# Optimization experiments

Hardware: AMD Instinct MI355X
Metric: run time of the kernel (lower is better)

The kernel has to match this reference:

```python
import jax, jax.numpy as jnp
import numpy as np

N = 1024
C = 50000
D = 128
M_MARGIN = 0.35
S_SCALE = 30.0
LAMDA = 0.01


def setup_inputs() -> dict:
    key = jax.random.key(0)
    k1, k2, k3 = jax.random.split(key, 3)
    feature = jax.random.normal(k1, (N, D), dtype=jnp.float32)
    weight = jax.random.normal(k2, (C, D), dtype=jnp.float32)
    label = jax.random.randint(k3, (N,), 0, C, dtype=jnp.int64)
    return {"feature": feature, "weight": weight, "label": label}


def reference(feature, weight, label):
    eps = 1e-8  # torch CosineSimilarity eps
    f = feature / jnp.maximum(jnp.linalg.norm(feature, axis=-1, keepdims=True), eps)
    w = weight / jnp.maximum(jnp.linalg.norm(weight, axis=-1, keepdims=True), eps)
    cos = jnp.einsum("nd,cd->nc", f, w)  # [N, C] cosine similarities
    onehot = jax.nn.one_hot(label, C, dtype=cos.dtype)  # [N, C]
    # CosFace: subtract margin m from the target-class cosine, scale by s
    logits = S_SCALE * (cos - M_MARGIN * onehot)
    target_logit = S_SCALE * (jnp.take_along_axis(cos, label[:, None], axis=1)[:, 0] - M_MARGIN)
    # -log( exp(t) / (exp(t) + sum_{j != y} exp(s*cos_j)) ) = logsumexp(logits) - t
    lse = jax.nn.logsumexp(logits, axis=-1)  # [N]
    loss_lmc = jnp.mean(lse - target_logit)
    # center loss: 0.5 * sum_i ||f_i - w_{y_i}||^2
    diff = feature - weight[label]
    loss_c = 0.5 * jnp.sum(diff * diff)
    return loss_lmc + LAMDA * loss_c
```

## Files before the change

kernel.cpp:

```cpp
#include <hip/hip_runtime.h>

#define N_ROWS   1024
#define D_DIM    128
#define C_CLS    50000
#define C_PAD    50048
#define NCT64    782
#define NG       96
#define NPART    192
#define S_SCALE  30.0f
#define M_MARGIN 0.35f
#define EXP2_SCALE 43.2808512266689f

typedef short s8v __attribute__((ext_vector_type(8)));
typedef float f4v __attribute__((ext_vector_type(4)));

__device__ inline unsigned short f2bf(float f) {
    unsigned u = __float_as_uint(f);
    u += 0x7FFF + ((u >> 16) & 1);
    return (unsigned short)(u >> 16);
}
__device__ inline float bf2f(unsigned short h) {
    return __uint_as_float(((unsigned)h) << 16);
}
__device__ inline void load_lds16(const char* src, unsigned char* lds) {
    __builtin_amdgcn_global_load_lds(
        (const __attribute__((address_space(1))) void*)src,
        (__attribute__((address_space(3))) void*)lds, 16, 0, 0);
}

__global__ void norm_rows_fused(const float* __restrict__ weight,
                                const float* __restrict__ feature,
                                unsigned short* __restrict__ what,
                                unsigned short* __restrict__ fhat) {
    int wid = threadIdx.x >> 6, lane = threadIdx.x & 63;
    int r = blockIdx.x * 4 + wid;
    const float* src;
    unsigned short* dst;
    int srcRow, valid;
    if (r < C_PAD) {
        src = weight; dst = what; srcRow = r; valid = (r < C_CLS);
    } else {
        src = feature; dst = fhat; srcRow = r - C_PAD; valid = 1;
    }
    float2 v = make_float2(0.f, 0.f);
    if (valid) v = ((const float2*)src)[(size_t)srcRow * 64 + lane];
    float ss = v.x * v.x + v.y * v.y;
    #pragma unroll
    for (int s = 1; s < 64; s <<= 1) ss += __shfl_xor(ss, s, 64);
    float inv = valid ? 1.0f / fmaxf(sqrtf(ss), 1e-8f) : 0.f;
    ((ushort2*)dst)[(size_t)srcRow * 64 + lane] =
        make_ushort2(f2bf(v.x * inv), f2bf(v.y * inv));
}

__global__ __launch_bounds__(256, 3)
void gemm_exp_kernel(const short* __restrict__ fhat,
                     const short* __restrict__ what,
                     float* __restrict__ part2) {
    __shared__ __align__(16) unsigned char smem[49152];
    const int g   = blockIdx.x;
    const int rt  = blockIdx.y;
    const int tid = threadIdx.x;
    const int wid = tid >> 6;
    const int lane = tid & 63;
    const int lrow = lane & 15;
    const int kgrp = lane >> 4;
    const int wrow = wid >> 1;
    const int wcol = wid & 1;
    const int nt = (g < 14) ? 9 : 8;

    const char* aSrc  = (const char*)fhat + (size_t)rt * 32768;
    const char* bBase = (const char*)what;

    #pragma unroll
    for (int i = 0; i < 8; i++) {
        int o = wid * 8192 + i * 1024 + lane * 16;
        int s = o ^ (((o >> 8) & 7) << 4);
        load_lds16(aSrc + s, smem + o);
    }
    __syncthreads();

    s8v afr[4][4];
    #pragma unroll
    for (int kk = 0; kk < 4; kk++)
        #pragma unroll
        for (int m = 0; m < 4; m++) {
            int row = wrow * 64 + m * 16 + lrow;
            int b = (row * 256 + kk * 64 + kgrp * 16) ^ ((row & 7) << 4);
            afr[kk][m] = *(const s8v*)(smem + b);
        }
    __syncthreads();

    #pragma unroll
    for (int i = 0; i < 4; i++) {
        int o = wid * 4096 + i * 1024 + lane * 16;
        int s = o ^ (((o >> 8) & 7) << 4);
        load_lds16(bBase + (size_t)g * 16384 + s, smem + o);
        load_lds16(bBase + (size_t)(g + 96) * 16384 + s, smem + 16384 + o);
    }

    float esum[4][4];
    #pragma unroll
    for (int m = 0; m < 4; m++)
        #pragma unroll
        for (int j = 0; j < 4; j++) esum[m][j] = 0.f;

    for (int t = 0; t < nt; ++t) {
        const int ct = g + 96 * t;
        if (t + 1 < nt) asm volatile("s_waitcnt vmcnt(4)" ::: "memory");
        else            asm volatile("s_waitcnt vmcnt(0)" ::: "memory");
        __builtin_amdgcn_s_barrier();
        __builtin_amdgcn_sched_barrier(0);

        if (t + 2 < nt) {
            const char* src = bBase + (size_t)(ct + 192) * 16384;
            unsigned char* dstb = smem + ((t + 2) % 3) * 16384;
            #pragma unroll
            for (int i = 0; i < 4; i++) {
                int o = wid * 4096 + i * 1024 + lane * 16;
                int s = o ^ (((o >> 8) & 7) << 4);
                load_lds16(src + s, dstb + o);
            }
        }

        const unsigned char* bb = smem + (t % 3) * 16384;
        f4v acc[4][2];
        f4v zero = {0.f, 0.f, 0.f, 0.f};
        #pragma unroll
        for (int m = 0; m < 4; m++) { acc[m][0] = zero; acc[m][1] = zero; }

        #pragma unroll
        for (int kk = 0; kk < 4; kk++) {
            s8v bfr[2];
            #pragma unroll
            for (int n = 0; n < 2; n++) {
                int row = wcol * 32 + n * 16 + lrow;
                int b = (row * 256 + kk * 64 + kgrp * 16) ^ ((row & 7) << 4);
                bfr[n] = *(const s8v*)(bb + b);
            }
            #pragma unroll
            for (int m = 0; m < 4; m++) {
                acc[m][0] = __builtin_amdgcn_mfma_f32_16x16x32_bf16(
                    afr[kk][m], bfr[0], acc[m][0], 0, 0, 0);
                acc[m][1] = __builtin_amdgcn_mfma_f32_16x16x32_bf16(
                    afr[kk][m], bfr[1], acc[m][1], 0, 0, 0);
            }
        }

        if (ct != NCT64 - 1) {
            #pragma unroll
            for (int m = 0; m < 4; m++)
                #pragma unroll
                for (int n = 0; n < 2; n++)
                    #pragma unroll
                    for (int j = 0; j < 4; j++)
                        esum[m][j] += __builtin_amdgcn_exp2f(EXP2_SCALE * acc[m][n][j]);
        } else {
            #pragma unroll
            for (int n = 0; n < 2; n++) {
                int gc = ct * 64 + wcol * 32 + n * 16 + lrow;
                #pragma unroll
                for (int m = 0; m < 4; m++)
                    #pragma unroll
                    for (int j = 0; j < 4; j++)
                        if (gc < C_CLS)
                            esum[m][j] += __builtin_amdgcn_exp2f(EXP2_SCALE * acc[m][n][j]);
            }
        }
    }

    #pragma unroll
    for (int m = 0; m < 4; m++)
        #pragma unroll
        for (int j = 0; j < 4; j++) {
            float v = esum[m][j];
            v += __shfl_xor(v, 1, 64);
            v += __shfl_xor(v, 2, 64);
            v += __shfl_xor(v, 4, 64);
            v += __shfl_xor(v, 8, 64);
            if (lrow == 0) {
                int row = rt * 128 + wrow * 64 + m * 16 + kgrp * 4 + j;
                part2[(size_t)row * NPART + g * 2 + wcol] = v;
            }
        }
}

__global__ void finalize_rows_kernel(const float* __restrict__ part2,
                                     const unsigned short* __restrict__ fhat,
                                     const unsigned short* __restrict__ what,
                                     const float* __restrict__ feature,
                                     const float* __restrict__ weight,
                                     const int* __restrict__ label,
                                     float* __restrict__ rowval) {
    int wid = threadIdx.x >> 6, lane = threadIdx.x & 63;
    int n = blockIdx.x * 4 + wid;
    int y = label[n];

    const float* p = part2 + (size_t)n * NPART;
    float S = p[lane] + p[64 + lane] + p[128 + lane];

    float2 f2 = ((const float2*)feature)[(size_t)n * 64 + lane];
    float2 w2 = ((const float2*)weight)[(size_t)y * 64 + lane];
    float dx = f2.x - w2.x, dy = f2.y - w2.y;
    float cl = dx * dx + dy * dy;

    ushort2 fh = ((const ushort2*)fhat)[(size_t)n * 64 + lane];
    ushort2 wh = ((const ushort2*)what)[(size_t)y * 64 + lane];
    float cy = bf2f(fh.x) * bf2f(wh.x) + bf2f(fh.y) * bf2f(wh.y);

    #pragma unroll
    for (int s = 1; s < 64; s <<= 1) {
        S  += __shfl_xor(S, s, 64);
        cl += __shfl_xor(cl, s, 64);
        cy += __shfl_xor(cy, s, 64);
    }
    if (lane == 0) {
        float t  = S_SCALE * (cy - M_MARGIN);
        float Sp = S - __expf(S_SCALE * cy) + __expf(t);
        rowval[n] = (logf(Sp) - t) * (1.0f / (float)N_ROWS) + 0.005f * cl;
    }
}

__global__ void reduce_final_kernel(const float* __restrict__ rowval, float* __restrict__ out) {
    __shared__ float sbuf[4];
    int t = threadIdx.x;
    float v = rowval[t] + rowval[t + 256] + rowval[t + 512] + rowval[t + 768];
    #pragma unroll
    for (int s = 1; s < 64; s <<= 1) v += __shfl_xor(v, s, 64);
    if ((t & 63) == 0) sbuf[t >> 6] = v;
    __syncthreads();
    if (t == 0) out[0] = sbuf[0] + sbuf[1] + sbuf[2] + sbuf[3];
}

extern "C" void kernel_launch(void* const* d_in, const int* in_sizes, int n_in,
                              void* d_out, int out_size, void* d_ws, size_t ws_size,
                              hipStream_t stream) {
    const float* feature = (const float*)d_in[0];
    const float* weight  = (const float*)d_in[1];
    const int*   label   = (const int*)d_in[2];

    const size_t WS_NEEDED = 13864960;
    if (ws_size < WS_NEEDED) return;

    char* ws = (char*)d_ws;
    unsigned short* what = (unsigned short*)ws;
    unsigned short* fhat = (unsigned short*)(ws + 12812288);
    float*         part2 = (float*)(ws + 13074432);
    float*        rowval = (float*)(ws + 13860864);

    norm_rows_fused<<<dim3((C_PAD + N_ROWS) / 4), 256, 0, stream>>>(weight, feature, what, fhat);
    gemm_exp_kernel<<<dim3(NG, 8), 256, 0, stream>>>((const short*)fhat, (const short*)what, part2);
    finalize_rows_kernel<<<dim3(N_ROWS / 4), 256, 0, stream>>>(part2, fhat, what, feature, weight,
                                                               label, rowval);
    reduce_final_kernel<<<1, 256, 0, stream>>>(rowval, (float*)d_out);
}
```

Before: 38.53 us.

## Widen GEMM grid to 128 groups with double buffering and prescaled features

The GEMM grid grows from 96 to 128 column groups, and the triple-buffered B pipeline with manual vmcnt waits becomes a double buffer using __syncthreads. This halves LDS from 48KB to 32KB, allowing occupancy 4 and more concurrent blocks. The exp2 scale is folded into the normalized features, removing a multiply per element, and the finalize step adapts to the scaled logits. The normalization kernel now handles two rows per wavefront using float4 loads. The trade-off is less prefetch depth (one tile ahead), which may expose memory latency.

```diff
diff --git a/kernel.cpp b/kernel.cpp
--- a/kernel.cpp
+++ b/kernel.cpp
@@ -5,11 +5,13 @@
 #define C_CLS    50000
 #define C_PAD    50048
 #define NCT64    782
-#define NG       96
-#define NPART    192
+#define NG       128
+#define NPART    256
 #define S_SCALE  30.0f
 #define M_MARGIN 0.35f
 #define EXP2_SCALE 43.2808512266689f
+#define EXP2M      15.1482979293341f
+#define LN2        0.6931471805599453f
 
 typedef short s8v __attribute__((ext_vector_type(8)));
 typedef float f4v __attribute__((ext_vector_type(4)));
@@ -33,30 +35,35 @@
                                 unsigned short* __restrict__ what,
                                 unsigned short* __restrict__ fhat) {
     int wid = threadIdx.x >> 6, lane = threadIdx.x & 63;
-    int r = blockIdx.x * 4 + wid;
+    int half = lane >> 5, l32 = lane & 31;
+    int r = blockIdx.x * 8 + wid * 2 + half;
+
     const float* src;
     unsigned short* dst;
     int srcRow, valid;
+    float scale;
     if (r < C_PAD) {
-        src = weight; dst = what; srcRow = r; valid = (r < C_CLS);
+        src = weight; dst = what; srcRow = r; valid = (r < C_CLS); scale = 1.0f;
     } else {
-        src = feature; dst = fhat; srcRow = r - C_PAD; valid = 1;
-    }
-    float2 v = make_float2(0.f, 0.f);
-    if (valid) v = ((const float2*)src)[(size_t)srcRow * 64 + lane];
-    float ss = v.x * v.x + v.y * v.y;
-    #pragma unroll
-    for (int s = 1; s < 64; s <<= 1) ss += __shfl_xor(ss, s, 64);
-    float inv = valid ? 1.0f / fmaxf(sqrtf(ss), 1e-8f) : 0.f;
-    ((ushort2*)dst)[(size_t)srcRow * 64 + lane] =
-        make_ushort2(f2bf(v.x * inv), f2bf(v.y * inv));
-}
-
-__global__ __launch_bounds__(256, 3)
+        src = feature; dst = fhat; srcRow = r - C_PAD; valid = 1; scale = EXP2_SCALE;
+    }
+    float4 v = make_float4(0.f, 0.f, 0.f, 0.f);
+    if (valid) v = ((const float4*)src)[(size_t)srcRow * 32 + l32];
+    float ss = v.x * v.x + v.y * v.y + v.z * v.z + v.w * v.w;
+    #pragma unroll
+    for (int s = 1; s < 32; s <<= 1) ss += __shfl_xor(ss, s, 32);
+    float inv = valid ? scale / fmaxf(sqrtf(ss), 1e-8f) : 0.f;
+    ushort4 o;
+    o.x = f2bf(v.x * inv); o.y = f2bf(v.y * inv);
+    o.z = f2bf(v.z * inv); o.w = f2bf(v.w * inv);
+    ((ushort4*)dst)[(size_t)srcRow * 32 + l32] = o;
+}
+
+__global__ __launch_bounds__(256, 4)
 void gemm_exp_kernel(const short* __restrict__ fhat,
                      const short* __restrict__ what,
                      float* __restrict__ part2) {
-    __shared__ __align__(16) unsigned char smem[49152];
+    __shared__ __align__(16) unsigned char smem[32768];
     const int g   = blockIdx.x;
     const int rt  = blockIdx.y;
     const int tid = threadIdx.x;
@@ -66,7 +73,7 @@
     const int kgrp = lane >> 4;
     const int wrow = wid >> 1;
     const int wcol = wid & 1;
-    const int nt = (g < 14) ? 9 : 8;
+    const int nt = (g < 14) ? 7 : 6;
 
     const char* aSrc  = (const char*)fhat + (size_t)rt * 32768;
     const char* bBase = (const char*)what;
@@ -95,7 +102,6 @@
         int o = wid * 4096 + i * 1024 + lane * 16;
         int s = o ^ (((o >> 8) & 7) << 4);
         load_lds16(bBase + (size_t)g * 16384 + s, smem + o);
-        load_lds16(bBase + (size_t)(g + 96) * 16384 + s, smem + 16384 + o);
     }
 
     float esum[4][4];
@@ -105,15 +111,12 @@
         for (int j = 0; j < 4; j++) esum[m][j] = 0.f;
 
     for (int t = 0; t < nt; ++t) {
-        const int ct = g + 96 * t;
-        if (t + 1 < nt) asm volatile("s_waitcnt vmcnt(4)" ::: "memory");
-        else            asm volatile("s_waitcnt vmcnt(0)" ::: "memory");
-        __builtin_amdgcn_s_barrier();
-        __builtin_amdgcn_sched_barrier(0);
-
-        if (t + 2 < nt) {
-            const char* src = bBase + (size_t)(ct + 192) * 16384;
-            unsigned char* dstb = smem + ((t + 2) % 3) * 16384;
+        const int ct = g + 128 * t;
+        __syncthreads();
+
+        if (t + 1 < nt) {
+            const char* src = bBase + (size_t)(ct + 128) * 16384;
+            unsigned char* dstb = smem + ((t + 1) & 1) * 16384;
             #pragma unroll
             for (int i = 0; i < 4; i++) {
                 int o = wid * 4096 + i * 1024 + lane * 16;
@@ -122,7 +125,7 @@
             }
         }
 
-        const unsigned char* bb = smem + (t % 3) * 16384;
+        const unsigned char* bb = smem + (t & 1) * 16384;
         f4v acc[4][2];
         f4v zero = {0.f, 0.f, 0.f, 0.f};
         #pragma unroll
@@ -153,7 +156,7 @@
                 for (int n = 0; n < 2; n++)
                     #pragma unroll
                     for (int j = 0; j < 4; j++)
-                        esum[m][j] += __builtin_amdgcn_exp2f(EXP2_SCALE * acc[m][n][j]);
+                        esum[m][j] += __builtin_amdgcn_exp2f(acc[m][n][j]);
         } else {
             #pragma unroll
             for (int n = 0; n < 2; n++) {
@@ -163,7 +166,7 @@
                     #pragma unroll
                     for (int j = 0; j < 4; j++)
                         if (gc < C_CLS)
-                            esum[m][j] += __builtin_amdgcn_exp2f(EXP2_SCALE * acc[m][n][j]);
+                            esum[m][j] += __builtin_amdgcn_exp2f(acc[m][n][j]);
             }
         }
     }
@@ -196,7 +199,7 @@
     int y = label[n];
 
     const float* p = part2 + (size_t)n * NPART;
-    float S = p[lane] + p[64 + lane] + p[128 + lane];
+    float S = p[lane] + p[64 + lane] + p[128 + lane] + p[192 + lane];
 
     float2 f2 = ((const float2*)feature)[(size_t)n * 64 + lane];
     float2 w2 = ((const float2*)weight)[(size_t)y * 64 + lane];
@@ -205,18 +208,18 @@
 
     ushort2 fh = ((const ushort2*)fhat)[(size_t)n * 64 + lane];
     ushort2 wh = ((const ushort2*)what)[(size_t)y * 64 + lane];
-    float cy = bf2f(fh.x) * bf2f(wh.x) + bf2f(fh.y) * bf2f(wh.y);
+    float cys = bf2f(fh.x) * bf2f(wh.x) + bf2f(fh.y) * bf2f(wh.y);
 
     #pragma unroll
     for (int s = 1; s < 64; s <<= 1) {
-        S  += __shfl_xor(S, s, 64);
-        cl += __shfl_xor(cl, s, 64);
-        cy += __shfl_xor(cy, s, 64);
+        S   += __shfl_xor(S, s, 64);
+        cl  += __shfl_xor(cl, s, 64);
+        cys += __shfl_xor(cys, s, 64);
     }
     if (lane == 0) {
-        float t  = S_SCALE * (cy - M_MARGIN);
-        float Sp = S - __expf(S_SCALE * cy) + __expf(t);
-        rowval[n] = (logf(Sp) - t) * (1.0f / (float)N_ROWS) + 0.005f * cl;
+        float t2 = cys - EXP2M;
+        float Sp = S - __builtin_amdgcn_exp2f(cys) + __builtin_amdgcn_exp2f(t2);
+        rowval[n] = (logf(Sp) - LN2 * t2) * (1.0f / (float)N_ROWS) + 0.005f * cl;
     }
 }
 
@@ -238,16 +241,16 @@
     const float* weight  = (const float*)d_in[1];
     const int*   label   = (const int*)d_in[2];
 
-    const size_t WS_NEEDED = 13864960;
+    const size_t WS_NEEDED = 14127104;
     if (ws_size < WS_NEEDED) return;
 
     char* ws = (char*)d_ws;
     unsigned short* what = (unsigned short*)ws;
     unsigned short* fhat = (unsigned short*)(ws + 12812288);
     float*         part2 = (float*)(ws + 13074432);
-    float*        rowval = (float*)(ws + 13860864);
-
-    norm_rows_fused<<<dim3((C_PAD + N_ROWS) / 4), 256, 0, stream>>>(weight, feature, what, fhat);
+    float*        rowval = (float*)(ws + 14123008);
+
+    norm_rows_fused<<<dim3((C_PAD + N_ROWS) / 8), 256, 0, stream>>>(weight, feature, what, fhat);
     gemm_exp_kernel<<<dim3(NG, 8), 256, 0, stream>>>((const short*)fhat, (const short*)what, part2);
     finalize_rows_kernel<<<dim3(N_ROWS / 4), 256, 0, stream>>>(part2, fhat, what, feature, weight,
                                                                label, rowval);
```

Result: slower. 63.96 us (+66.0%).
